# Kernel optimization log

Measured on AMD Instinct MI355X. Metric: run time of the kernel, lower is better.

Reference implementation:

```python
import jax, jax.numpy as jnp
from jax import lax
import numpy as np

VOCAB, EDIM, HID, NCLS, OC = 30000, 300, 256, 20, 32
T_TXT = 32
HW = 224


def setup_inputs() -> dict:
    key = jax.random.key(0)
    ks = jax.random.split(key, 18)
    g = lambda i, shape, s=0.05: jax.random.normal(ks[i], shape, jnp.float32) * s
    n_videos, n_seg, seg_frames, seg_records = 4, 4, 16, 15
    total_f = n_videos * n_seg * seg_frames          # 256 frames
    n_rec = n_videos * n_seg * seg_records           # 240 text records
    return {
        "image_input": jax.random.normal(ks[0], (total_f, 3, HW, HW), jnp.float32),
        "text_input": jax.random.randint(ks[1], (n_rec, T_TXT), 0, VOCAB),
        "text_lens": jax.random.randint(ks[2], (n_rec,), 1, T_TXT + 1),
        "n_videos": n_videos, "n_seg": n_seg,
        "seg_frames": seg_frames, "seg_records": seg_records,
        "emb": g(3, (VOCAB, EDIM), 1.0),
        "Wih_l0": g(4, (2, 4 * HID, EDIM)), "Whh_l0": g(5, (2, 4 * HID, HID)),
        "bih_l0": g(6, (2, 4 * HID)), "bhh_l0": g(7, (2, 4 * HID)),
        "Wih_l1": g(8, (2, 4 * HID, 2 * HID)), "Whh_l1": g(9, (2, 4 * HID, HID)),
        "bih_l1": g(10, (2, 4 * HID)), "bhh_l1": g(11, (2, 4 * HID)),
        "conv_w": g(12, (OC, 3, 3, 7, 7)), "conv_b": g(13, (OC,)),
        "lin_w": g(14, (NCLS, 2 * HID + 14 * 14 * OC)), "lin_b": g(15, (NCLS,)),
    }


def _lstm_dir(x, mask_t, Wih, Whh, bih, bhh, reverse):
    # x: [B,T,D]; mask_t: [T,B,1]. Torch LSTM gate order: i,f,g,o.
    B, T, _ = x.shape
    H = Whh.shape[1]
    pre = jnp.einsum('btd,gd->btg', x, Wih) + bih + bhh  # [B,T,4H]

    def step(carry, inp):
        h, c = carry
        g, m = inp
        z = g + h @ Whh.T
        i, f, cc, o = jnp.split(z, 4, -1)
        c_new = jax.nn.sigmoid(f) * c + jax.nn.sigmoid(i) * jnp.tanh(cc)
        h_new = jax.nn.sigmoid(o) * jnp.tanh(c_new)
        # packed-sequence semantics: state frozen and output zero at pads
        return (jnp.where(m, h_new, h), jnp.where(m, c_new, c)), jnp.where(m, h_new, 0.0)

    init = (jnp.zeros((B, H), x.dtype), jnp.zeros((B, H), x.dtype))
    _, out = lax.scan(step, init, (jnp.swapaxes(pre, 0, 1), mask_t), reverse=reverse)
    return jnp.swapaxes(out, 0, 1)  # [B,T,H]


def reference(image_input, text_input, text_lens, n_videos, n_seg, seg_frames,
              seg_records, emb, Wih_l0, Whh_l0, bih_l0, bhh_l0, Wih_l1, Whh_l1,
              bih_l1, bhh_l1, conv_w, conv_b, lin_w, lin_b):
    V, fpv = int(n_videos), int(n_seg) * int(seg_frames)
    total_f = V * fpv
    # ---- CNN3D branch: pad_sequence is a no-op for uniform video lengths ----
    x = image_input.reshape(V, fpv, 3, HW, HW)
    x = jnp.swapaxes(x, 1, 2)  # [V,3,F,H,W]
    conv = lax.conv_general_dilated(
        x, conv_w, (1, 2, 2), [(1, 1), (3, 3), (3, 3)],
        dimension_numbers=('NCDHW', 'OIDHW', 'NCDHW')) + conv_b[None, :, None, None, None]
    pool = lax.reduce_window(conv, -jnp.inf, lax.max, (1, 1, 3, 8, 8), (1, 1, 1, 8, 8),
                             ((0, 0), (0, 0), (1, 1), (0, 0), (0, 0)))  # [V,OC,F,14,14]
    frames = jnp.moveaxis(pool, 2, 1).reshape(total_f, OC, 14, 14)  # cat over videos, [total_f,OC,14,14]
    adj = (frames[:-1] + frames[1:]) * 0.5
    # static boolean mask removing cross-segment adjacent pairs
    seg = np.full((V, int(n_seg)), int(seg_frames), np.int64)
    offs = np.arange(V) * fpv
    bnd = (np.cumsum(seg, 1) + offs[:, None] - 1).ravel()[:-1]
    keep = np.ones(total_f - 1, bool)
    keep[bnd] = False
    image_avg = adj[keep].reshape(int(keep.sum()), -1)  # [N_rec, OC*196]

    # ---- text branch: embedding + 2-layer BiLSTM with masked mean ----
    h = emb[text_input]  # [N,T,E]
    mask = jnp.arange(T_TXT)[None, :] < text_lens[:, None]  # [N,T]
    mask_t = jnp.swapaxes(mask, 0, 1)[..., None]
    for Wih, Whh, bih, bhh in ((Wih_l0, Whh_l0, bih_l0, bhh_l0),
                               (Wih_l1, Whh_l1, bih_l1, bhh_l1)):
        fwd = _lstm_dir(h, mask_t, Wih[0], Whh[0], bih[0], bhh[0], reverse=False)
        bwd = _lstm_dir(h, mask_t, Wih[1], Whh[1], bih[1], bhh[1], reverse=True)
        h = jnp.concatenate([fwd, bwd], -1)
    rnn_avg = (h * mask[..., None]).sum(1) / text_lens[:, None].astype(h.dtype)

    # ---- fuse, classify, per-video max over records ----
    logits = jnp.concatenate([image_avg, rnn_avg], -1) @ lin_w.T + lin_b
    scores = jax.nn.sigmoid(logits)
    rec_per_video = int(n_seg) * int(seg_records)
    return scores.reshape(V, rec_per_video, NCLS).max(axis=1)
```

## Files before the change

### kernel.cpp

```cpp
#include <hip/hip_runtime.h>
#include <math.h>

#define NV 4
#define NREC 240
#define TT 32
#define EDIM 300
#define HID 256
#define G4 1024
#define OC 32
#define NCLS 20
#define IMGF 6272
#define FEATD 6784
#define NROW 7680
#define IMG_PIX 50176

typedef __attribute__((ext_vector_type(8))) short short8;
typedef __attribute__((ext_vector_type(16))) float floatx16;
typedef __attribute__((ext_vector_type(2))) _Float16 h2;
typedef unsigned short u16;

__device__ inline u16 f2bf(float x) {
    unsigned int u = __float_as_uint(x);
    unsigned int r = u + 0x7FFFu + ((u >> 16) & 1u);
    return (u16)(r >> 16);
}

__global__ void prep_wmfma_kernel(const float* __restrict__ cw, u16* __restrict__ wprep) {
    int idx = blockIdx.x * 256 + threadIdx.x;
    if (idx >= 64 * 32 * 8) return;
    int q  = idx & 7;
    int oc = (idx >> 3) & 31;
    int r  = idx >> 8;
    float v = 0.f;
    if (r < 63 && q < 7) {
        int pl = r / 7, kw = r % 7;
        int c = pl / 3, kd = pl % 3;
        v = cw[(size_t)oc * 441 + c * 147 + kd * 49 + q * 7 + kw];
    }
    wprep[idx] = f2bf(v);
}

__global__ void prep_whhH_kernel(const float* __restrict__ w0, const float* __restrict__ w1,
                                 _Float16* __restrict__ whhH) {
    int idx = blockIdx.x * 256 + threadIdx.x;
    int p  = idx & 1;
    int g  = (idx >> 1) & 3;
    int hu = (idx >> 3) & 255;
    int k2 = (idx >> 11) & 127;
    int d  = (idx >> 18) & 1;
    int l  = (idx >> 19) & 1;
    const float* W = l ? w1 : w0;
    whhH[idx] = (_Float16)W[((size_t)d * G4 + g * 256 + hu) * 256 + k2 * 2 + p];
}

__global__ void prep_wihb_kernel(const float* __restrict__ src, u16* __restrict__ dst,
                                 int K, int Kp) {
    int idx = blockIdx.x * 256 + threadIdx.x;
    if (idx >= 2 * 1024 * Kp) return;
    int k = idx % Kp;
    int j = idx / Kp;
    dst[idx] = (k < K) ? f2bf(src[(size_t)j * K + k]) : (u16)0;
}

#define REG_PITCH 1840
#define PLANE_PITCH 3680
#define WOFF 33120
#define CONV_LDS_TOTAL (33120 + 63 * 512)

template<int RL>
__device__ __attribute__((always_inline))
static void conv_mfma_pass(const unsigned char* lds, int xe, int half, int m, floatx16& acc) {
#pragma unroll
    for (int kk = 0; kk < 32; ++kk) {
        int r = kk * 2 + half;
        int pl = r / 7;
        int kw = r - pl * 7;
        bool pad = (pl > 8);
        if (pad) { pl = 8; kw = 6; }
        int reg = (kw + 1) & 1;
        int hw  = (kw + 1) >> 1;
        short8 af = *(const short8*)(lds + pl * PLANE_PITCH + reg * REG_PITCH + (xe + hw) * 16);
        int rcl = pad ? 0 : r;
        short8 canon = *(const short8*)(lds + WOFF + rcl * 512 + m * 16);
        if (pad) { short8 z = {0,0,0,0,0,0,0,0}; canon = z; }
        short8 bfr = __builtin_shufflevector(canon, canon,
            (RL)&7, (RL+1)&7, (RL+2)&7, (RL+3)&7, (RL+4)&7, (RL+5)&7, (RL+6)&7, (RL+7)&7);
        acc = __builtin_amdgcn_mfma_f32_32x32x16_bf16(af, bfr, acc, 0, 0, 0);
    }
}

__global__ __launch_bounds__(256) void conv_pool_kernel(
    const float* __restrict__ img,
    const u16* __restrict__ wprep,
    const float* __restrict__ cb,
    float* __restrict__ spool)
{
    __shared__ __align__(16) unsigned char lds[CONV_LDS_TOTAL];
    int blk = blockIdx.x;
    int hh = blk & 1;
    int vf = blk >> 1;
    int f  = vf & 63;
    int tid  = threadIdx.x;
    int lane = tid & 63;
    int wv   = tid >> 6;
    int m    = lane & 31;
    int half = lane >> 5;
    int x  = wv * 32 + m;
    int xe = x > 111 ? 111 : x;

    {
        const uint4* wp4 = (const uint4*)wprep;
        uint4* wl4 = (uint4*)(lds + WOFF);
        for (int k0 = tid; k0 < 2016; k0 += 256) wl4[k0] = wp4[k0];
    }

    int u = tid & 127;
    int rowsel = tid >> 7;
    int y0 = 56 * hh;

    for (int rnd = 0; rnd < 4; ++rnd) {
        int zz = 2 * y0 - 3 + 2 * rnd + rowsel;
        bool force0 = (2 * rnd + rowsel) == 7;
        int zc = zz < 0 ? 0 : (zz > 223 ? 223 : zz);
        bool zok = ((unsigned)zz < 224u) && !force0;
        int col = 2 * u - 4;
        int colc = col < 0 ? 0 : (col > 222 ? 222 : col);
        bool uok = (u >= 2 && u <= 113);
        if (u < 115) {
            int slot = (zz + 16) & 7;
#pragma unroll 1
            for (int p = 0; p < 9; ++p) {
                int c = p / 3, kd = p - c * 3;
                int zf = f + kd - 1;
                int zp = vf + kd - 1;
                int zpc = zp < 0 ? 0 : (zp > 255 ? 255 : zp);
                bool ok = zok && uok && (0 <= zf) && (zf < 64);
                float2 pv = *(const float2*)(img + ((size_t)zpc * 3 + c) * IMG_PIX
                                             + (size_t)zc * 224 + colc);
                float vx = ok ? pv.x : 0.f, vy = ok ? pv.y : 0.f;
                unsigned char* ldp = lds + p * PLANE_PITCH;
                *(u16*)(ldp + u * 16 + slot * 2) = f2bf(vx);
                *(u16*)(ldp + REG_PITCH + u * 16 + slot * 2) = f2bf(vy);
            }
        }
    }
    __syncthreads();

    float pmax[4];
    for (int y = y0; y < y0 + 56; ++y) {
        int dy = y & 7;
        if (dy == 0) {
#pragma unroll
            for (int rc = 0; rc < 4; ++rc) pmax[rc] = -3.0e38f;
        }
        int zz = 2 * y + 4 + rowsel;
        int zc = zz > 223 ? 223 : zz;
        bool zok = zz <= 223;
        int col = 2 * u - 4;
        int colc = col < 0 ? 0 : (col > 222 ? 222 : col);
        bool uok = (u >= 2 && u <= 113);
        float2 pf[9];
#pragma unroll
        for (int p = 0; p < 9; ++p) {
            int c = p / 3, kd = p - c * 3;
            int zp = vf + kd - 1;
            int zpc = zp < 0 ? 0 : (zp > 255 ? 255 : zp);
            pf[p] = *(const float2*)(img + ((size_t)zpc * 3 + c) * IMG_PIX
                                     + (size_t)zc * 224 + colc);
        }
        floatx16 acc = {0,0,0,0,0,0,0,0,0,0,0,0,0,0,0,0};
        switch (y & 3) {
            case 0: conv_mfma_pass<3>(lds, xe, half, m, acc); break;
            case 1: conv_mfma_pass<1>(lds, xe, half, m, acc); break;
            case 2: conv_mfma_pass<7>(lds, xe, half, m, acc); break;
            default: conv_mfma_pass<5>(lds, xe, half, m, acc); break;
        }
#pragma unroll
        for (int z = 0; z < 16; ++z)
            pmax[z >> 2] = fmaxf(pmax[z >> 2], acc[z]);
        if (dy == 7) {
#pragma unroll
            for (int rc = 0; rc < 4; ++rc)
                pmax[rc] = fmaxf(pmax[rc], __shfl_xor(pmax[rc], 32, 64));
            if (half == 0) {
                float bias = cb[m];
                int i = y >> 3;
#pragma unroll
                for (int rc = 0; rc < 4; ++rc) {
                    int jc = wv * 4 + rc;
                    if (jc < 14)
                        spool[((size_t)vf * 196 + i * 14 + jc) * 32 + m] = pmax[rc] + bias;
                }
            }
        }
        __syncthreads();
        if (u < 115) {
            int slot = (zz + 16) & 7;
#pragma unroll 1
            for (int p = 0; p < 9; ++p) {
                int c = p / 3, kd = p - c * 3;
                int zf = f + kd - 1;
                bool ok = zok && uok && (0 <= zf) && (zf < 64);
                float vx = ok ? pf[p].x : 0.f, vy = ok ? pf[p].y : 0.f;
                unsigned char* ldp = lds + p * PLANE_PITCH;
                *(u16*)(ldp + u * 16 + slot * 2) = f2bf(vx);
                *(u16*)(ldp + REG_PITCH + u * 16 + slot * 2) = f2bf(vy);
            }
        }
        __syncthreads();
    }
}

__global__ void depth_adj_kernel(const float* __restrict__ spool, float* __restrict__ feat) {
    int idx = blockIdx.x * 256 + threadIdx.x;
    if (idx >= NREC * IMGF) return;
    int col = idx % IMGF;
    int r   = idx / IMGF;
    int o  = col / 196, ij = col % 196;
    int g  = r / 15, jj = r % 15;
    int tt = 16 * g + jj;
    int v  = tt >> 6, f = tt & 63;
    const int FS = 196 * 32;
    const float* S = spool + ((size_t)(v * 64) * 196 + ij) * 32 + o;
    float a = S[(size_t)f * FS];
    if (f > 0) a = fmaxf(a, S[(size_t)(f - 1) * FS]);
    a = fmaxf(a, S[(size_t)(f + 1) * FS]);
    int f2 = f + 1;
    float b = fmaxf(S[(size_t)f2 * FS], S[(size_t)(f2 - 1) * FS]);
    if (f2 + 1 < 64) b = fmaxf(b, S[(size_t)(f2 + 1) * FS]);
    feat[(size_t)r * FEATD + col] = 0.5f * (a + b);
}

__global__ void embed_bf_kernel(const int* __restrict__ txt, const float* __restrict__ emb,
                                u16* __restrict__ x0b) {
    int idx = blockIdx.x * 256 + threadIdx.x;
    if (idx >= NROW * 320) return;
    int e = idx % 320, nt = idx / 320;
    x0b[idx] = (e < EDIM) ? f2bf(emb[(size_t)txt[nt] * EDIM + e]) : (u16)0;
}

#define PGP 40
__global__ __launch_bounds__(256) void pregate_mfma(
    const u16* __restrict__ A,
    const u16* __restrict__ W,
    const float* __restrict__ b1, const float* __restrict__ b2,
    float* __restrict__ out, int Kp)
{
    __shared__ __align__(16) u16 a_s[128 * PGP];
    __shared__ __align__(16) u16 b_s[128 * PGP];
    int d  = blockIdx.z;
    int m0 = blockIdx.x * 128;
    int j0 = blockIdx.y * 128;
    const u16* Wd = W + (size_t)d * G4 * Kp;
    float* outd = out + (size_t)d * NROW * G4;
    int tid = threadIdx.x;
    int lane = tid & 63;
    int wv = tid >> 6;
    int wm = wv & 1, wn = wv >> 1;
    int ln31 = lane & 31, lh = lane >> 5;
    floatx16 acc[2][2];
#pragma unroll
    for (int a = 0; a < 2; a++)
#pragma unroll
        for (int b = 0; b < 2; b++) {
            floatx16 z = {0,0,0,0,0,0,0,0,0,0,0,0,0,0,0,0};
            acc[a][b] = z;
        }
    for (int k0 = 0; k0 < Kp; k0 += 32) {
#pragma unroll
        for (int li = 0; li < 2; li++) {
            int e = tid + li * 256;
            int row = e >> 2, part = e & 3;
            uint4 va = *(const uint4*)(A + (size_t)(m0 + row) * Kp + k0 + part * 8);
            *(uint4*)&a_s[row * PGP + part * 8] = va;
            uint4 vb = *(const uint4*)(Wd + (size_t)(j0 + row) * Kp + k0 + part * 8);
            *(uint4*)&b_s[row * PGP + part * 8] = vb;
        }
        __syncthreads();
#pragma unroll
        for (int kk = 0; kk < 2; kk++) {
            int ko = kk * 16 + lh * 8;
            short8 a0 = *(const short8*)&a_s[(wm * 64 + ln31) * PGP + ko];
            short8 a1 = *(const short8*)&a_s[(wm * 64 + 32 + ln31) * PGP + ko];
            short8 b0 = *(const short8*)&b_s[(wn * 64 + ln31) * PGP + ko];
            short8 b1v = *(const short8*)&b_s[(wn * 64 + 32 + ln31) * PGP + ko];
            acc[0][0] = __builtin_amdgcn_mfma_f32_32x32x16_bf16(a0, b0, acc[0][0], 0, 0, 0);
            acc[0][1] = __builtin_amdgcn_mfma_f32_32x32x16_bf16(a0, b1v, acc[0][1], 0, 0, 0);
            acc[1][0] = __builtin_amdgcn_mfma_f32_32x32x16_bf16(a1, b0, acc[1][0], 0, 0, 0);
            acc[1][1] = __builtin_amdgcn_mfma_f32_32x32x16_bf16(a1, b1v, acc[1][1], 0, 0, 0);
        }
        __syncthreads();
    }
#pragma unroll
    for (int mi = 0; mi < 2; mi++)
#pragma unroll
        for (int ni = 0; ni < 2; ni++) {
#pragma unroll
            for (int rg = 0; rg < 16; rg++) {
                int row = m0 + wm * 64 + mi * 32 + (rg & 3) + 8 * (rg >> 2) + 4 * lh;
                int colj = j0 + wn * 64 + ni * 32 + ln31;
                outd[(size_t)row * G4 + colj] =
                    acc[mi][ni][rg] + b1[d * G4 + colj] + b2[d * G4 + colj];
            }
        }
}

__global__ __launch_bounds__(256) void lstm_kernel(
    const float* __restrict__ pre,
    const _Float16* __restrict__ whh,
    const int* __restrict__ lens,
    float* __restrict__ houtf,
    u16* __restrict__ houtb,
    int obf)
{
    int d  = blockIdx.y;
    int n0 = blockIdx.x * 3;
    int hu = threadIdx.x;
    __shared__ __align__(16) _Float16 hs[2][3][256];
    float h[3] = {0.f, 0.f, 0.f}, c[3] = {0.f, 0.f, 0.f};
    int len[3] = {lens[n0], lens[n0 + 1], lens[n0 + 2]};
    hs[0][0][hu] = (_Float16)0.f; hs[0][1][hu] = (_Float16)0.f; hs[0][2][hu] = (_Float16)0.f;
    __syncthreads();
    int cur = 0;
    const _Float16* wb = whh + (size_t)d * 262144;
    const float* preb = pre + (size_t)d * NROW * G4;
    for (int ss = 0; ss < 32; ss++) {
        int t = d ? (31 - ss) : ss;
        float ai[3], af[3], ag[3], ao[3];
#pragma unroll
        for (int b = 0; b < 3; b++) {
            const float* pp = preb + ((size_t)(n0 + b) * TT + t) * G4 + hu;
            ai[b] = pp[0]; af[b] = pp[256]; ag[b] = pp[512]; ao[b] = pp[768];
        }
#pragma unroll 4
        for (int k2 = 0; k2 < 128; k2++) {
            uint4 wr = *(const uint4*)(wb + ((size_t)k2 * 256 + hu) * 8);
            h2 wi = __builtin_bit_cast(h2, wr.x);
            h2 wf = __builtin_bit_cast(h2, wr.y);
            h2 wg = __builtin_bit_cast(h2, wr.z);
            h2 wo = __builtin_bit_cast(h2, wr.w);
#pragma unroll
            for (int b = 0; b < 3; b++) {
                h2 hv = *(const h2*)&hs[cur][b][2 * k2];
#if __has_builtin(__builtin_amdgcn_fdot2)
                ai[b] = __builtin_amdgcn_fdot2(wi, hv, ai[b], false);
                af[b] = __builtin_amdgcn_fdot2(wf, hv, af[b], false);
                ag[b] = __builtin_amdgcn_fdot2(wg, hv, ag[b], false);
                ao[b] = __builtin_amdgcn_fdot2(wo, hv, ao[b], false);
#else
                ai[b] += (float)wi.x * (float)hv.x + (float)wi.y * (float)hv.y;
                af[b] += (float)wf.x * (float)hv.x + (float)wf.y * (float)hv.y;
                ag[b] += (float)wg.x * (float)hv.x + (float)wg.y * (float)hv.y;
                ao[b] += (float)wo.x * (float)hv.x + (float)wo.y * (float)hv.y;
#endif
            }
        }
        int nxt = cur ^ 1;
#pragma unroll
        for (int b = 0; b < 3; b++) {
            float iv = 1.f / (1.f + expf(-ai[b]));
            float fv = 1.f / (1.f + expf(-af[b]));
            float gv = tanhf(ag[b]);
            float ov = 1.f / (1.f + expf(-ao[b]));
            float cn = fmaf(fv, c[b], iv * gv);
            float hn = ov * tanhf(cn);
            bool mk = t < len[b];
            float outv = mk ? hn : 0.f;
            if (mk) { c[b] = cn; h[b] = hn; }
            size_t oidx = ((size_t)(n0 + b) * TT + t) * 512 + d * 256 + hu;
            if (obf) houtb[oidx] = f2bf(outv);
            else     houtf[oidx] = outv;
            hs[nxt][b][hu] = (_Float16)h[b];
        }
        __syncthreads();
        cur = nxt;
    }
}

__global__ void rnn_avg_kernel(const float* __restrict__ h1, const int* __restrict__ lens,
                               float* __restrict__ feat) {
    int idx = blockIdx.x * 256 + threadIdx.x;
    if (idx >= NREC * 512) return;
    int n = idx >> 9, cd = idx & 511;
    float s = 0.f;
    for (int t = 0; t < TT; t++) s += h1[((size_t)n * TT + t) * 512 + cd];
    feat[(size_t)n * FEATD + IMGF + cd] = s / (float)lens[n];
}

__global__ __launch_bounds__(256) void final_kernel(const float* __restrict__ feat,
                                                    const float* __restrict__ lw,
                                                    const float* __restrict__ lb,
                                                    float* __restrict__ scores) {
    int n = blockIdx.x;
    float acc[NCLS];
#pragma unroll
    for (int cc = 0; cc < NCLS; cc++) acc[cc] = 0.f;
    for (int k = threadIdx.x; k < FEATD; k += 256) {
        float fv = feat[(size_t)n * FEATD + k];
#pragma unroll
        for (int cc = 0; cc < NCLS; cc++)
            acc[cc] = fmaf(fv, lw[cc * FEATD + k], acc[cc]);
    }
#pragma unroll
    for (int cc = 0; cc < NCLS; cc++) {
#pragma unroll
        for (int off = 32; off >= 1; off >>= 1)
            acc[cc] += __shfl_xor(acc[cc], off, 64);
    }
    __shared__ float red[NCLS][4];
    int lane = threadIdx.x & 63, wid = threadIdx.x >> 6;
    if (lane == 0)
        for (int cc = 0; cc < NCLS; cc++) red[cc][wid] = acc[cc];
    __syncthreads();
    if (threadIdx.x < NCLS) {
        float s = red[threadIdx.x][0] + red[threadIdx.x][1] + red[threadIdx.x][2] +
                  red[threadIdx.x][3] + lb[threadIdx.x];
        scores[n * NCLS + threadIdx.x] = 1.f / (1.f + expf(-s));
    }
}

__global__ void vidmax_kernel(const float* __restrict__ scores, float* __restrict__ out) {
    int idx = threadIdx.x;
    if (idx < NV * NCLS) {
        int v = idx / NCLS, cc = idx % NCLS;
        float m = -3.0e38f;
        for (int r = 0; r < 60; r++)
            m = fmaxf(m, scores[(v * 60 + r) * NCLS + cc]);
        out[idx] = m;
    }
}

extern "C" void kernel_launch(void* const* d_in, const int* in_sizes, int n_in,
                              void* d_out, int out_size, void* d_ws, size_t ws_size,
                              hipStream_t stream) {
    (void)in_sizes; (void)n_in; (void)out_size; (void)ws_size;
    const float* img  = (const float*)d_in[0];
    const int*   txt  = (const int*)d_in[1];
    const int*   lens = (const int*)d_in[2];
    const float* emb  = (const float*)d_in[7];
    const float* Wih0 = (const float*)d_in[8];
    const float* Whh0 = (const float*)d_in[9];
    const float* bih0 = (const float*)d_in[10];
    const float* bhh0 = (const float*)d_in[11];
    const float* Wih1 = (const float*)d_in[12];
    const float* Whh1 = (const float*)d_in[13];
    const float* bih1 = (const float*)d_in[14];
    const float* bhh1 = (const float*)d_in[15];
    const float* cw   = (const float*)d_in[16];
    const float* cb   = (const float*)d_in[17];
    const float* lw   = (const float*)d_in[18];
    const float* lb   = (const float*)d_in[19];

    char* wsb = (char*)d_ws;
    u16*      wprep = (u16*)wsb;
    _Float16* whhH  = (_Float16*)(wsb + 32768);
    u16*      wihb0 = (u16*)(wsb + 2129920);
    u16*      wihb1 = (u16*)(wsb + 3440640);
    u16*      x0b   = (u16*)(wsb + 5537792);
    float*    pre   = (float*)(wsb + 10452992);
    u16*      h0b   = (u16*)(wsb + 73367552);
    float*    h1o   = (float*)(wsb + 81231872);
    float*    spool = (float*)(wsb + 96960512);
    float*    feat  = (float*)(wsb + 103383040);
    float*    scor  = (float*)(wsb + 109895680);

    prep_wmfma_kernel<<<64, 256, 0, stream>>>(cw, wprep);
    prep_whhH_kernel<<<4096, 256, 0, stream>>>(Whh0, Whh1, whhH);
    prep_wihb_kernel<<<2560, 256, 0, stream>>>(Wih0, wihb0, 300, 320);
    prep_wihb_kernel<<<4096, 256, 0, stream>>>(Wih1, wihb1, 512, 512);
    conv_pool_kernel<<<512, 256, 0, stream>>>(img, wprep, cb, spool);
    depth_adj_kernel<<<5880, 256, 0, stream>>>(spool, feat);
    embed_bf_kernel<<<9600, 256, 0, stream>>>(txt, emb, x0b);
    pregate_mfma<<<dim3(60, 8, 2), 256, 0, stream>>>(x0b, wihb0, bih0, bhh0, pre, 320);
    lstm_kernel<<<dim3(80, 2), 256, 0, stream>>>(pre, whhH, lens, h1o, h0b, 1);
    pregate_mfma<<<dim3(60, 8, 2), 256, 0, stream>>>(h0b, wihb1, bih1, bhh1, pre, 512);
    lstm_kernel<<<dim3(80, 2), 256, 0, stream>>>(pre, whhH + 524288, lens, h1o, h0b, 0);
    rnn_avg_kernel<<<480, 256, 0, stream>>>(h1o, lens, feat);
    final_kernel<<<240, 256, 0, stream>>>(feat, lw, lb, scor);
    vidmax_kernel<<<1, 128, 0, stream>>>(scor, (float*)d_out);
}
```

Measured before the change: 1.159 ms.

## Keep conv weight fragments in registers and merge weight-prep kernels

The conv weight B-fragments (32 short8 per lane) are preloaded into registers once per block instead of being staged in LDS and re-read every row, which shrinks LDS and adds a launch_bounds occupancy hint of 2 blocks. The weight rotation is folded into the prep layout so the per-row shuffle offset changes, and the y loop is unrolled by 4 to make the shuffle pattern compile-time. The four weight-prep kernels are fused into one launch to cut launch overhead. The cost is higher register pressure (128 VGPRs of weights) and a possible risk of spills.

```diff
diff --git a/kernel.cpp b/kernel.cpp
--- a/kernel.cpp
+++ b/kernel.cpp
@@ -25,51 +25,74 @@
     return (u16)(r >> 16);
 }
 
-__global__ void prep_wmfma_kernel(const float* __restrict__ cw, u16* __restrict__ wprep) {
+__global__ void prep_all_kernel(const float* __restrict__ cw,
+                                const float* __restrict__ w0, const float* __restrict__ w1,
+                                const float* __restrict__ wih0, const float* __restrict__ wih1,
+                                u16* __restrict__ wprep, _Float16* __restrict__ whhH,
+                                u16* __restrict__ wihb0, u16* __restrict__ wihb1) {
     int idx = blockIdx.x * 256 + threadIdx.x;
-    if (idx >= 64 * 32 * 8) return;
-    int q  = idx & 7;
-    int oc = (idx >> 3) & 31;
-    int r  = idx >> 8;
-    float v = 0.f;
-    if (r < 63 && q < 7) {
-        int pl = r / 7, kw = r % 7;
-        int c = pl / 3, kd = pl % 3;
-        v = cw[(size_t)oc * 441 + c * 147 + kd * 49 + q * 7 + kw];
-    }
-    wprep[idx] = f2bf(v);
-}
-
-__global__ void prep_whhH_kernel(const float* __restrict__ w0, const float* __restrict__ w1,
-                                 _Float16* __restrict__ whhH) {
-    int idx = blockIdx.x * 256 + threadIdx.x;
-    int p  = idx & 1;
-    int g  = (idx >> 1) & 3;
-    int hu = (idx >> 3) & 255;
-    int k2 = (idx >> 11) & 127;
-    int d  = (idx >> 18) & 1;
-    int l  = (idx >> 19) & 1;
-    const float* W = l ? w1 : w0;
-    whhH[idx] = (_Float16)W[((size_t)d * G4 + g * 256 + hu) * 256 + k2 * 2 + p];
-}
-
-__global__ void prep_wihb_kernel(const float* __restrict__ src, u16* __restrict__ dst,
-                                 int K, int Kp) {
-    int idx = blockIdx.x * 256 + threadIdx.x;
-    if (idx >= 2 * 1024 * Kp) return;
-    int k = idx % Kp;
-    int j = idx / Kp;
-    dst[idx] = (k < K) ? f2bf(src[(size_t)j * K + k]) : (u16)0;
+    {
+        int p  = idx & 1;
+        int g  = (idx >> 1) & 3;
+        int hu = (idx >> 3) & 255;
+        int k2 = (idx >> 11) & 127;
+        int d  = (idx >> 18) & 1;
+        int l  = (idx >> 19) & 1;
+        const float* W = l ? w1 : w0;
+        whhH[idx] = (_Float16)W[((size_t)d * G4 + g * 256 + hu) * 256 + k2 * 2 + p];
+    }
+    wihb1[idx] = f2bf(wih1[idx]);
+    if (idx < 2 * 1024 * 320) {
+        int k = idx % 320;
+        int j = idx / 320;
+        wihb0[idx] = (k < 300) ? f2bf(wih0[(size_t)j * 300 + k]) : (u16)0;
+    }
+    if (idx < 64 * 32 * 8) {
+        int qd = idx & 7;
+        int oc = (idx >> 3) & 31;
+        int r  = idx >> 8;
+        int kh = (qd + 1) & 7;
+        float v = 0.f;
+        if (r < 63 && kh < 7) {
+            int pl = r / 7, kw = r % 7;
+            int c = pl / 3, kd = pl % 3;
+            v = cw[(size_t)oc * 441 + c * 147 + kd * 49 + kh * 7 + kw];
+        }
+        wprep[idx] = f2bf(v);
+    }
 }
 
 #define REG_PITCH 1840
 #define PLANE_PITCH 3680
-#define WOFF 33120
-#define CONV_LDS_TOTAL (33120 + 63 * 512)
-
-template<int RL>
+#define CONV_LDS_TOTAL 33120
+
+template<int E>
 __device__ __attribute__((always_inline))
-static void conv_mfma_pass(const unsigned char* lds, int xe, int half, int m, floatx16& acc) {
+static void conv_y_body(int y, unsigned char* lds, const float* __restrict__ img,
+                        const short8* Bc, const float* __restrict__ cb,
+                        float* __restrict__ spool, float* pmax,
+                        int vf, int f, int u, int rowsel, int xe, int half, int m, int wv)
+{
+    if ((y & 7) == 0) {
+#pragma unroll
+        for (int rc = 0; rc < 4; ++rc) pmax[rc] = -3.0e38f;
+    }
+    int zz = 2 * y + 4 + rowsel;
+    int zc = zz > 223 ? 223 : zz;
+    bool zok = zz <= 223;
+    int col = 2 * u - 4;
+    int colc = col < 0 ? 0 : (col > 222 ? 222 : col);
+    bool uok = (u >= 2 && u <= 113);
+    float2 pf[9];
+#pragma unroll
+    for (int p = 0; p < 9; ++p) {
+        int c = p / 3, kd = p - c * 3;
+        int zp = vf + kd - 1;
+        int zpc = zp < 0 ? 0 : (zp > 255 ? 255 : zp);
+        pf[p] = *(const float2*)(img + ((size_t)zpc * 3 + c) * IMG_PIX
+                                 + (size_t)zc * 224 + colc);
+    }
+    floatx16 acc = {0,0,0,0,0,0,0,0,0,0,0,0,0,0,0,0};
 #pragma unroll
     for (int kk = 0; kk < 32; ++kk) {
         int r = kk * 2 + half;
@@ -80,16 +103,47 @@
         int reg = (kw + 1) & 1;
         int hw  = (kw + 1) >> 1;
         short8 af = *(const short8*)(lds + pl * PLANE_PITCH + reg * REG_PITCH + (xe + hw) * 16);
-        int rcl = pad ? 0 : r;
-        short8 canon = *(const short8*)(lds + WOFF + rcl * 512 + m * 16);
-        if (pad) { short8 z = {0,0,0,0,0,0,0,0}; canon = z; }
-        short8 bfr = __builtin_shufflevector(canon, canon,
-            (RL)&7, (RL+1)&7, (RL+2)&7, (RL+3)&7, (RL+4)&7, (RL+5)&7, (RL+6)&7, (RL+7)&7);
+        short8 b = Bc[kk];
+        short8 bfr = __builtin_shufflevector(b, b,
+            (0+E)&7, (1+E)&7, (2+E)&7, (3+E)&7, (4+E)&7, (5+E)&7, (6+E)&7, (7+E)&7);
         acc = __builtin_amdgcn_mfma_f32_32x32x16_bf16(af, bfr, acc, 0, 0, 0);
     }
-}
-
-__global__ __launch_bounds__(256) void conv_pool_kernel(
+#pragma unroll
+    for (int z = 0; z < 16; ++z)
+        pmax[z >> 2] = fmaxf(pmax[z >> 2], acc[z]);
+    if ((y & 7) == 7) {
+#pragma unroll
+        for (int rc = 0; rc < 4; ++rc)
+            pmax[rc] = fmaxf(pmax[rc], __shfl_xor(pmax[rc], 32, 64));
+        if (half == 0) {
+            float bias = cb[m];
+            int i = y >> 3;
+#pragma unroll
+            for (int rc = 0; rc < 4; ++rc) {
+                int jc = wv * 4 + rc;
+                if (jc < 14)
+                    spool[((size_t)vf * 196 + i * 14 + jc) * 32 + m] = pmax[rc] + bias;
+            }
+        }
+    }
+    __syncthreads();
+    if (u < 115) {
+        int slot = (zz + 16) & 7;
+#pragma unroll 1
+        for (int p = 0; p < 9; ++p) {
+            int c = p / 3, kd = p - c * 3;
+            int zf = f + kd - 1;
+            bool ok = zok && uok && (0 <= zf) && (zf < 64);
+            float vx = ok ? pf[p].x : 0.f, vy = ok ? pf[p].y : 0.f;
+            unsigned char* ldp = lds + p * PLANE_PITCH;
+            *(u16*)(ldp + u * 16 + slot * 2) = f2bf(vx);
+            *(u16*)(ldp + REG_PITCH + u * 16 + slot * 2) = f2bf(vy);
+        }
+    }
+    __syncthreads();
+}
+
+__global__ __launch_bounds__(256, 2) void conv_pool_kernel(
     const float* __restrict__ img,
     const u16* __restrict__ wprep,
     const float* __restrict__ cb,
@@ -108,11 +162,10 @@
     int x  = wv * 32 + m;
     int xe = x > 111 ? 111 : x;
 
-    {
-        const uint4* wp4 = (const uint4*)wprep;
-        uint4* wl4 = (uint4*)(lds + WOFF);
-        for (int k0 = tid; k0 < 2016; k0 += 256) wl4[k0] = wp4[k0];
-    }
+    short8 Bc[32];
+#pragma unroll
+    for (int kk = 0; kk < 32; ++kk)
+        Bc[kk] = *(const short8*)(wprep + (((size_t)(2 * kk + half) * 32 + m) << 3));
 
     int u = tid & 127;
     int rowsel = tid >> 7;
@@ -147,67 +200,12 @@
     __syncthreads();
 
     float pmax[4];
-    for (int y = y0; y < y0 + 56; ++y) {
-        int dy = y & 7;
-        if (dy == 0) {
-#pragma unroll
-            for (int rc = 0; rc < 4; ++rc) pmax[rc] = -3.0e38f;
-        }
-        int zz = 2 * y + 4 + rowsel;
-        int zc = zz > 223 ? 223 : zz;
-        bool zok = zz <= 223;
-        int col = 2 * u - 4;
-        int colc = col < 0 ? 0 : (col > 222 ? 222 : col);
-        bool uok = (u >= 2 && u <= 113);
-        float2 pf[9];
-#pragma unroll
-        for (int p = 0; p < 9; ++p) {
-            int c = p / 3, kd = p - c * 3;
-            int zp = vf + kd - 1;
-            int zpc = zp < 0 ? 0 : (zp > 255 ? 255 : zp);
-            pf[p] = *(const float2*)(img + ((size_t)zpc * 3 + c) * IMG_PIX
-                                     + (size_t)zc * 224 + colc);
-        }
-        floatx16 acc = {0,0,0,0,0,0,0,0,0,0,0,0,0,0,0,0};
-        switch (y & 3) {
-            case 0: conv_mfma_pass<3>(lds, xe, half, m, acc); break;
-            case 1: conv_mfma_pass<1>(lds, xe, half, m, acc); break;
-            case 2: conv_mfma_pass<7>(lds, xe, half, m, acc); break;
-            default: conv_mfma_pass<5>(lds, xe, half, m, acc); break;
-        }
-#pragma unroll
-        for (int z = 0; z < 16; ++z)
-            pmax[z >> 2] = fmaxf(pmax[z >> 2], acc[z]);
-        if (dy == 7) {
-#pragma unroll
-            for (int rc = 0; rc < 4; ++rc)
-                pmax[rc] = fmaxf(pmax[rc], __shfl_xor(pmax[rc], 32, 64));
-            if (half == 0) {
-                float bias = cb[m];
-                int i = y >> 3;
-#pragma unroll
-                for (int rc = 0; rc < 4; ++rc) {
-                    int jc = wv * 4 + rc;
-                    if (jc < 14)
-                        spool[((size_t)vf * 196 + i * 14 + jc) * 32 + m] = pmax[rc] + bias;
-                }
-            }
-        }
-        __syncthreads();
-        if (u < 115) {
-            int slot = (zz + 16) & 7;
-#pragma unroll 1
-            for (int p = 0; p < 9; ++p) {
-                int c = p / 3, kd = p - c * 3;
-                int zf = f + kd - 1;
-                bool ok = zok && uok && (0 <= zf) && (zf < 64);
-                float vx = ok ? pf[p].x : 0.f, vy = ok ? pf[p].y : 0.f;
-                unsigned char* ldp = lds + p * PLANE_PITCH;
-                *(u16*)(ldp + u * 16 + slot * 2) = f2bf(vx);
-                *(u16*)(ldp + REG_PITCH + u * 16 + slot * 2) = f2bf(vy);
-            }
-        }
-        __syncthreads();
+    for (int yq = 0; yq < 14; ++yq) {
+        int yb = y0 + yq * 4;
+        conv_y_body<2>(yb + 0, lds, img, Bc, cb, spool, pmax, vf, f, u, rowsel, xe, half, m, wv);
+        conv_y_body<0>(yb + 1, lds, img, Bc, cb, spool, pmax, vf, f, u, rowsel, xe, half, m, wv);
+        conv_y_body<6>(yb + 2, lds, img, Bc, cb, spool, pmax, vf, f, u, rowsel, xe, half, m, wv);
+        conv_y_body<4>(yb + 3, lds, img, Bc, cb, spool, pmax, vf, f, u, rowsel, xe, half, m, wv);
     }
 }
 
@@ -464,10 +462,8 @@
     float*    feat  = (float*)(wsb + 103383040);
     float*    scor  = (float*)(wsb + 109895680);
 
-    prep_wmfma_kernel<<<64, 256, 0, stream>>>(cw, wprep);
-    prep_whhH_kernel<<<4096, 256, 0, stream>>>(Whh0, Whh1, whhH);
-    prep_wihb_kernel<<<2560, 256, 0, stream>>>(Wih0, wihb0, 300, 320);
-    prep_wihb_kernel<<<4096, 256, 0, stream>>>(Wih1, wihb1, 512, 512);
+    prep_all_kernel<<<4096, 256, 0, stream>>>(cw, Whh0, Whh1, Wih0, Wih1,
+                                              wprep, whhH, wihb0, wihb1);
     conv_pool_kernel<<<512, 256, 0, stream>>>(img, wprep, cb, spool);
     depth_adj_kernel<<<5880, 256, 0, stream>>>(spool, feat);
     embed_bf_kernel<<<9600, 256, 0, stream>>>(txt, emb, x0b);
```

Measured after the change: 1.954 ms. 68.5% more time.
